# Kernel optimization log

Hardware: AMD Instinct MI355X
Metric: run time of the kernel (lower is better)

## Reference

```python
import jax, jax.numpy as jnp
import numpy as np

# Quantization constants from the original module
X_ZP = -66   # int8 zero point
Y_ZP = 160   # uint8 zero point


def setup_inputs() -> dict:
    key = jax.random.key(0)
    k1, k2 = jax.random.split(key)
    # x: [7, B, M, K] int8 in [-128, 127]
    x = jax.random.randint(k1, (7, 8, 512, 1024), -128, 128, dtype=jnp.int32).astype(jnp.int8)
    # y: [B, K, N] uint8 in [0, 255]
    y = jax.random.randint(k2, (8, 1024, 512), 0, 256, dtype=jnp.int32).astype(jnp.uint8)
    return {
        "x": x,
        "y": y,
        "x_scale": jnp.float32(0.03),
        "y_scale": jnp.float32(0.025),
    }


def reference(x, y, x_scale, y_scale):
    # dequantize_per_tensor: (q - zero_point) * scale
    xf = (x.astype(jnp.float32) - jnp.float32(X_ZP)) * x_scale   # [7, B, M, K]
    yf = (y.astype(jnp.float32) - jnp.float32(Y_ZP)) * y_scale   # [B, K, N]
    # torch.matmul broadcast: [7,B,M,K] @ [B,K,N] -> [7,B,M,N]
    return jnp.einsum('gbmk,bkn->gbmn', xf, yf)
```

## Files before the change

### kernel.cpp

```cpp
#include <hip/hip_runtime.h>
#include <stdint.h>

#define AS1 __attribute__((address_space(1)))
#define AS3 __attribute__((address_space(3)))

typedef int v4i __attribute__((ext_vector_type(4)));

constexpr int G = 7, B = 8, M = 512, N = 512, K = 1024;
constexpr int GBn = G * B;

constexpr size_t YT_BYTES = (size_t)B * N * K;
constexpr size_t CSP_CNT  = (size_t)16 * B * N;
constexpr size_t WS_NEEDED = YT_BYTES + CSP_CNT * 4;

__global__ __launch_bounds__(256) void transpose_pack_y(const int* __restrict__ y,
                                                        signed char* __restrict__ yt,
                                                        int* __restrict__ csp) {
    __shared__ unsigned char tile[64][80];
    int n0  = blockIdx.x * 64;
    int k0t = blockIdx.y;
    int k0  = k0t * 64;
    int b   = blockIdx.z;
    int t   = threadIdx.x;

    int r  = t >> 2;
    int c0 = (t & 3) * 16;
    const int* src = y + ((size_t)b * K + k0 + r) * N + n0 + c0;
    uint32_t p[4];
#pragma unroll
    for (int q = 0; q < 4; ++q) {
        int4 v = ((const int4*)src)[q];
        p[q] =  (uint32_t)((v.x & 255) ^ 128)
             | ((uint32_t)((v.y & 255) ^ 128) << 8)
             | ((uint32_t)((v.z & 255) ^ 128) << 16)
             | ((uint32_t)((v.w & 255) ^ 128) << 24);
    }
    *(uint4*)&tile[r][c0] = make_uint4(p[0], p[1], p[2], p[3]);
    __syncthreads();

    int nl = t >> 2;
    int kc = (t & 3) * 16;
    uint32_t q[4];
    int s = 0;
#pragma unroll
    for (int w = 0; w < 4; ++w) {
        uint32_t b0 = tile[kc + w * 4 + 0][nl];
        uint32_t b1 = tile[kc + w * 4 + 1][nl];
        uint32_t b2 = tile[kc + w * 4 + 2][nl];
        uint32_t b3 = tile[kc + w * 4 + 3][nl];
        s += (int)(signed char)b0 + (int)(signed char)b1
           + (int)(signed char)b2 + (int)(signed char)b3;
        q[w] = b0 | (b1 << 8) | (b2 << 16) | (b3 << 24);
    }
    *(uint4*)(yt + ((size_t)b * N + n0 + nl) * K + k0 + kc) = make_uint4(q[0], q[1], q[2], q[3]);

    s += __shfl_xor(s, 1, 64);
    s += __shfl_xor(s, 2, 64);
    if ((t & 3) == 0) csp[(size_t)k0t * (B * N) + b * N + n0 + nl] = s;
}

__global__ __launch_bounds__(512, 2) void gemm_fused(const int* __restrict__ x,
                                                     const signed char* __restrict__ yt,
                                                     const int* __restrict__ csp,
                                                     const float* __restrict__ xsp,
                                                     const float* __restrict__ ysp,
                                                     float* __restrict__ out) {
    __shared__ __align__(16) signed char As[2][128 * 64];
    __shared__ __align__(16) signed char Bs[2][512 * 64];
    __shared__ int cs_lds[512];
    __shared__ int rs_lds[128];

    int id  = blockIdx.x;
    int swz = (id & 7) * 28 + (id >> 3);
    int gb  = swz >> 2;
    int mt  = swz & 3;
    int b   = gb & 7;

    int tid = threadIdx.x, wave = tid >> 6, lane = tid & 63;

    {
        int s = 0;
        const int* p = csp + b * N + tid;
#pragma unroll
        for (int kt = 0; kt < 16; ++kt) s += p[(size_t)kt * (B * N)];
        cs_lds[tid] = s;
    }

    int arow = tid >> 2;
    int akq  = tid & 3;
    const int4* Asrc = (const int4*)(x + ((size_t)(gb * M + mt * 128 + arow)) * K) + akq * 4;
    int aoff = arow * 64 + ((akq ^ ((arow >> 1) & 3)) << 4);

    int brl    = lane >> 2;
    int bchunk = (lane & 3) ^ ((lane >> 3) & 3);
    const signed char* Bsrc = yt + ((size_t)b * N) * K;

    int fr = lane & 15;
    int fk = ((lane >> 4) ^ ((fr >> 1) & 3)) << 4;
    int wm = (wave >> 2) * 64;
    int wn = (wave & 3) * 128;

    v4i zero = {0, 0, 0, 0};
    v4i acc[4][8];
#pragma unroll
    for (int i = 0; i < 4; ++i)
#pragma unroll
        for (int j = 0; j < 8; ++j) acc[i][j] = zero;

    int rsum = 0;

    int4 av[4];
#pragma unroll
    for (int q = 0; q < 4; ++q) av[q] = Asrc[q];
#pragma unroll
    for (int c = 0; c < 4; ++c) {
        __builtin_amdgcn_global_load_lds(
            (const AS1 uint32_t*)(Bsrc + (size_t)(c * 128 + wave * 16 + brl) * K + bchunk * 16),
            (AS3 uint32_t*)(&Bs[0][(c * 128 + wave * 16) * 64]), 16, 0, 0);
    }

#pragma unroll 2
    for (int t = 0; t < 16; ++t) {
        int cur = t & 1;

        uint32_t pw[4];
        int s = 0;
#pragma unroll
        for (int q = 0; q < 4; ++q) {
            int4 v = av[q];
            s += v.x + v.y + v.z + v.w;
            pw[q] =  (uint32_t)(v.x & 255)
                 | ((uint32_t)(v.y & 255) << 8)
                 | ((uint32_t)(v.z & 255) << 16)
                 | ((uint32_t)(v.w & 255) << 24);
        }
        rsum += s;
        *(uint4*)(&As[cur][aoff]) = make_uint4(pw[0], pw[1], pw[2], pw[3]);

        __syncthreads();

        v4i af[4], bf[8];
#pragma unroll
        for (int i = 0; i < 4; ++i)
            af[i] = *(const v4i*)(&As[cur][(wm + i * 16 + fr) * 64 + fk]);
#pragma unroll
        for (int j = 0; j < 8; ++j)
            bf[j] = *(const v4i*)(&Bs[cur][(wn + j * 16 + fr) * 64 + fk]);

        if (t < 15) {
#pragma unroll
            for (int q = 0; q < 4; ++q) av[q] = Asrc[(t + 1) * 16 + q];
#pragma unroll
            for (int c = 0; c < 4; ++c) {
                __builtin_amdgcn_global_load_lds(
                    (const AS1 uint32_t*)(Bsrc + (size_t)(c * 128 + wave * 16 + brl) * K
                                          + (t + 1) * 64 + bchunk * 16),
                    (AS3 uint32_t*)(&Bs[cur ^ 1][(c * 128 + wave * 16) * 64]), 16, 0, 0);
            }
        }

#pragma unroll
        for (int i = 0; i < 4; ++i)
#pragma unroll
            for (int j = 0; j < 8; ++j)
                acc[i][j] = __builtin_amdgcn_mfma_i32_16x16x64_i8(af[i], bf[j], acc[i][j], 0, 0, 0);
    }

    rsum += __shfl_xor(rsum, 1, 64);
    rsum += __shfl_xor(rsum, 2, 64);
    if ((tid & 3) == 0) rs_lds[arow] = rsum;
    __syncthreads();

    float sc = xsp[0] * ysp[0];
    int colL = lane & 15;
    int rowQ = (lane >> 4) * 4;
    float* outg = out + (size_t)gb * (M * N) + (size_t)(mt * 128) * N;
#pragma unroll
    for (int i = 0; i < 4; ++i) {
#pragma unroll
        for (int r = 0; r < 4; ++r) {
            int row_l = wm + i * 16 + rowQ + r;
            int rsv = rs_lds[row_l];
#pragma unroll
            for (int j = 0; j < 8; ++j) {
                int col = wn + j * 16 + colL;
                int tv = acc[i][j][r] - 32 * rsv + 66 * cs_lds[col] - 2162688;
                outg[(size_t)row_l * N + col] = sc * (float)tv;
            }
        }
    }
}

__global__ __launch_bounds__(256) void naive_kernel(const int* __restrict__ x,
                                                    const int* __restrict__ y,
                                                    const float* __restrict__ xsp,
                                                    const float* __restrict__ ysp,
                                                    float* __restrict__ out) {
    size_t idx = (size_t)blockIdx.x * 256 + threadIdx.x;
    int n  = (int)(idx & 511);
    int m  = (int)((idx >> 9) & 511);
    int gb = (int)(idx >> 18);
    int b  = gb & 7;
    const int* xr = x + ((size_t)gb * M + m) * K;
    const int* yc = y + (size_t)b * K * N + n;
    int dot = 0, sx = 0, sy = 0;
    for (int k = 0; k < K; ++k) {
        int a = xr[k];
        int c = yc[(size_t)k * N];
        dot += a * c; sx += a; sy += c;
    }
    float s = xsp[0] * ysp[0];
    out[idx] = s * (float)(dot - 160 * sx + 66 * sy - 10813440);
}

extern "C" void kernel_launch(void* const* d_in, const int* in_sizes, int n_in,
                              void* d_out, int out_size, void* d_ws, size_t ws_size,
                              hipStream_t stream) {
    const int*   x  = (const int*)d_in[0];
    const int*   y  = (const int*)d_in[1];
    const float* xs = (const float*)d_in[2];
    const float* ys = (const float*)d_in[3];
    float* out = (float*)d_out;

    if (ws_size < WS_NEEDED) {
        naive_kernel<<<(14680064 + 255) / 256, 256, 0, stream>>>(x, y, xs, ys, out);
        return;
    }

    char* ws = (char*)d_ws;
    signed char* yt  = (signed char*)ws;
    int*         csp = (int*)(ws + YT_BYTES);

    transpose_pack_y<<<dim3(N / 64, K / 64, B), 256, 0, stream>>>(y, yt, csp);
    gemm_fused<<<dim3(224), 512, 0, stream>>>(x, yt, csp, xs, ys, out);
}
```

Before: 216.7 us.

## Pre-pack int32 x to int8 with row sums, stream A via async LDS loads

Adds a pack_x kernel that narrows the int32-stored x to int8 and computes per-row sums into workspace. The GEMM then loads A tiles with global_load_lds, the same async path B already uses, instead of loading int32 into registers and packing them each K step. LDS fragment reads move after the prefetch issue. The aim is to drop per-iteration ALU packing and synchronous register loads from the main loop. The cost is an extra launch and an extra write and read of the packed x.

```diff
diff --git a/kernel.cpp b/kernel.cpp
--- a/kernel.cpp
+++ b/kernel.cpp
@@ -9,9 +9,11 @@
 constexpr int G = 7, B = 8, M = 512, N = 512, K = 1024;
 constexpr int GBn = G * B;
 
+constexpr size_t X8_BYTES = (size_t)GBn * M * K;
 constexpr size_t YT_BYTES = (size_t)B * N * K;
 constexpr size_t CSP_CNT  = (size_t)16 * B * N;
-constexpr size_t WS_NEEDED = YT_BYTES + CSP_CNT * 4;
+constexpr size_t RS_CNT   = (size_t)GBn * M;
+constexpr size_t WS_NEEDED = X8_BYTES + YT_BYTES + CSP_CNT * 4 + RS_CNT * 4;
 
 __global__ __launch_bounds__(256) void transpose_pack_y(const int* __restrict__ y,
                                                         signed char* __restrict__ yt,
@@ -59,16 +61,39 @@
     if ((t & 3) == 0) csp[(size_t)k0t * (B * N) + b * N + n0 + nl] = s;
 }
 
-__global__ __launch_bounds__(512, 2) void gemm_fused(const int* __restrict__ x,
-                                                     const signed char* __restrict__ yt,
-                                                     const int* __restrict__ csp,
-                                                     const float* __restrict__ xsp,
-                                                     const float* __restrict__ ysp,
-                                                     float* __restrict__ out) {
+__global__ __launch_bounds__(256) void pack_x(const int* __restrict__ x,
+                                              signed char* __restrict__ x8,
+                                              int* __restrict__ rowsum) {
+    int wave = threadIdx.x >> 6, lane = threadIdx.x & 63;
+    int row = blockIdx.x * 4 + wave;
+    const int4* src = (const int4*)(x + (size_t)row * K) + lane * 4;
+    int s = 0;
+    uint32_t p[4];
+#pragma unroll
+    for (int q = 0; q < 4; ++q) {
+        int4 v = src[q];
+        s += v.x + v.y + v.z + v.w;
+        p[q] =  (uint32_t)(v.x & 255)
+             | ((uint32_t)(v.y & 255) << 8)
+             | ((uint32_t)(v.z & 255) << 16)
+             | ((uint32_t)(v.w & 255) << 24);
+    }
+    *(uint4*)(x8 + (size_t)row * K + lane * 16) = make_uint4(p[0], p[1], p[2], p[3]);
+#pragma unroll
+    for (int off = 32; off > 0; off >>= 1) s += __shfl_down(s, off, 64);
+    if (lane == 0) rowsum[row] = s;
+}
+
+__global__ __launch_bounds__(512, 2) void gemm_i8(const signed char* __restrict__ x8,
+                                                  const signed char* __restrict__ yt,
+                                                  const int* __restrict__ rowsum,
+                                                  const int* __restrict__ csp,
+                                                  const float* __restrict__ xsp,
+                                                  const float* __restrict__ ysp,
+                                                  float* __restrict__ out) {
     __shared__ __align__(16) signed char As[2][128 * 64];
     __shared__ __align__(16) signed char Bs[2][512 * 64];
     __shared__ int cs_lds[512];
-    __shared__ int rs_lds[128];
 
     int id  = blockIdx.x;
     int swz = (id & 7) * 28 + (id >> 3);
@@ -86,10 +111,9 @@
         cs_lds[tid] = s;
     }
 
-    int arow = tid >> 2;
-    int akq  = tid & 3;
-    const int4* Asrc = (const int4*)(x + ((size_t)(gb * M + mt * 128 + arow)) * K) + akq * 4;
-    int aoff = arow * 64 + ((akq ^ ((arow >> 1) & 3)) << 4);
+    int srow   = lane >> 2;
+    int schunk = (lane & 3) ^ ((lane >> 3) & 3);
+    const signed char* Asrc = x8 + ((size_t)(gb * M + mt * 128 + wave * 16 + srow)) * K + schunk * 16;
 
     int brl    = lane >> 2;
     int bchunk = (lane & 3) ^ ((lane >> 3) & 3);
@@ -107,11 +131,8 @@
 #pragma unroll
         for (int j = 0; j < 8; ++j) acc[i][j] = zero;
 
-    int rsum = 0;
-
-    int4 av[4];
-#pragma unroll
-    for (int q = 0; q < 4; ++q) av[q] = Asrc[q];
+    __builtin_amdgcn_global_load_lds((const AS1 uint32_t*)(Asrc),
+                                     (AS3 uint32_t*)(&As[0][wave * 1024]), 16, 0, 0);
 #pragma unroll
     for (int c = 0; c < 4; ++c) {
         __builtin_amdgcn_global_load_lds(
@@ -123,33 +144,12 @@
     for (int t = 0; t < 16; ++t) {
         int cur = t & 1;
 
-        uint32_t pw[4];
-        int s = 0;
-#pragma unroll
-        for (int q = 0; q < 4; ++q) {
-            int4 v = av[q];
-            s += v.x + v.y + v.z + v.w;
-            pw[q] =  (uint32_t)(v.x & 255)
-                 | ((uint32_t)(v.y & 255) << 8)
-                 | ((uint32_t)(v.z & 255) << 16)
-                 | ((uint32_t)(v.w & 255) << 24);
-        }
-        rsum += s;
-        *(uint4*)(&As[cur][aoff]) = make_uint4(pw[0], pw[1], pw[2], pw[3]);
-
         __syncthreads();
 
-        v4i af[4], bf[8];
-#pragma unroll
-        for (int i = 0; i < 4; ++i)
-            af[i] = *(const v4i*)(&As[cur][(wm + i * 16 + fr) * 64 + fk]);
-#pragma unroll
-        for (int j = 0; j < 8; ++j)
-            bf[j] = *(const v4i*)(&Bs[cur][(wn + j * 16 + fr) * 64 + fk]);
-
         if (t < 15) {
-#pragma unroll
-            for (int q = 0; q < 4; ++q) av[q] = Asrc[(t + 1) * 16 + q];
+            __builtin_amdgcn_global_load_lds(
+                (const AS1 uint32_t*)(Asrc + (t + 1) * 64),
+                (AS3 uint32_t*)(&As[cur ^ 1][wave * 1024]), 16, 0, 0);
 #pragma unroll
             for (int c = 0; c < 4; ++c) {
                 __builtin_amdgcn_global_load_lds(
@@ -159,28 +159,32 @@
             }
         }
 
+        v4i af[4], bf[8];
+#pragma unroll
+        for (int i = 0; i < 4; ++i)
+            af[i] = *(const v4i*)(&As[cur][(wm + i * 16 + fr) * 64 + fk]);
+#pragma unroll
+        for (int j = 0; j < 8; ++j)
+            bf[j] = *(const v4i*)(&Bs[cur][(wn + j * 16 + fr) * 64 + fk]);
+
 #pragma unroll
         for (int i = 0; i < 4; ++i)
 #pragma unroll
             for (int j = 0; j < 8; ++j)
                 acc[i][j] = __builtin_amdgcn_mfma_i32_16x16x64_i8(af[i], bf[j], acc[i][j], 0, 0, 0);
     }
-
-    rsum += __shfl_xor(rsum, 1, 64);
-    rsum += __shfl_xor(rsum, 2, 64);
-    if ((tid & 3) == 0) rs_lds[arow] = rsum;
-    __syncthreads();
 
     float sc = xsp[0] * ysp[0];
     int colL = lane & 15;
     int rowQ = (lane >> 4) * 4;
     float* outg = out + (size_t)gb * (M * N) + (size_t)(mt * 128) * N;
+    const int* rs = rowsum + gb * M + mt * 128;
 #pragma unroll
     for (int i = 0; i < 4; ++i) {
 #pragma unroll
         for (int r = 0; r < 4; ++r) {
             int row_l = wm + i * 16 + rowQ + r;
-            int rsv = rs_lds[row_l];
+            int rsv = rs[row_l];
 #pragma unroll
             for (int j = 0; j < 8; ++j) {
                 int col = wn + j * 16 + colL;
@@ -228,9 +232,12 @@
     }
 
     char* ws = (char*)d_ws;
-    signed char* yt  = (signed char*)ws;
-    int*         csp = (int*)(ws + YT_BYTES);
+    signed char* x8  = (signed char*)ws;
+    signed char* yt  = (signed char*)(ws + X8_BYTES);
+    int*         csp = (int*)(ws + X8_BYTES + YT_BYTES);
+    int*         rsm = csp + CSP_CNT;
 
     transpose_pack_y<<<dim3(N / 64, K / 64, B), 256, 0, stream>>>(y, yt, csp);
-    gemm_fused<<<dim3(224), 512, 0, stream>>>(x, yt, csp, xs, ys, out);
-}
+    pack_x<<<GBn * M / 4, 256, 0, stream>>>(x, x8, rsm);
+    gemm_i8<<<dim3(224), 512, 0, stream>>>(x8, yt, rsm, csp, xs, ys, out);
+}
```

New measurement: 230.8 us. 6.5% more time.
